# Performance work log

Hardware: AMD Instinct MI355X
Metric: run time of the kernel (lower is better)

The kernel has to match this reference:

```python
import jax, jax.numpy as jnp
import numpy as np

N, E = 50000, 400000
C_IN, C_OUT = 64, 32
K = 9  # kernel_size 3x3


def _quad_basis(t):
    # open B-spline basis, degree 2, per torch_spline_conv: k_mod in {0,1,2}
    # t = frac(pseudo * (kernel_size - degree)) = pseudo here (kernel_size=3, degree=2)
    return jnp.stack([0.5 * (1.0 - t) ** 2, -t * t + t + 0.5, 0.5 * t * t], axis=-1)  # [E,3]


def spline_basis(pseudo):
    # kernel_size=[3,3], degree=2, open spline: v = p*(3-2)=p, floor(v)=0 for p in [0,1),
    # so weight index for combination s is exactly s = k_mod0 + 3*k_mod1.
    q0 = _quad_basis(pseudo[:, 0])  # [E,3] varies with s%3
    q1 = _quad_basis(pseudo[:, 1])  # [E,3] varies with s//3
    return (q1[:, :, None] * q0[:, None, :]).reshape(-1, K)  # [E,9]


def spline_conv(x, src, dst, B, W, root, bias, n_nodes):
    xj = x[src]  # gather source node features [E,Cin]
    msg = jnp.zeros((xj.shape[0], W.shape[-1]), x.dtype)
    for k in range(K):  # fixed small kernel loop; avoids [E,K,Cin] blowup
        msg = msg + (xj * B[:, k, None]) @ W[k]
    agg = jax.ops.segment_sum(msg, dst, num_segments=n_nodes)  # aggr='add'
    return agg + x @ root + bias


def setup_inputs() -> dict:
    key = jax.random.key(0)
    ks = jax.random.split(key, 10)
    x = jax.random.normal(ks[0], (N, C_IN), jnp.float32)
    edge_index = jax.random.randint(ks[1], (2, E), 0, N, jnp.int64)
    pseudo = jax.random.uniform(ks[2], (E, 2), jnp.float32)
    skip = jax.random.normal(ks[3], (N, C_OUT), jnp.float32)
    s1 = 1.0 / np.sqrt(C_IN)
    s2 = 1.0 / np.sqrt(C_OUT)
    W1 = jax.random.normal(ks[4], (K, C_IN, C_OUT), jnp.float32) * s1
    root1 = jax.random.normal(ks[5], (C_IN, C_OUT), jnp.float32) * s1
    b1 = jnp.zeros((C_OUT,), jnp.float32)
    W2 = jax.random.normal(ks[6], (K, C_OUT, C_OUT), jnp.float32) * s2
    root2 = jax.random.normal(ks[7], (C_OUT, C_OUT), jnp.float32) * s2
    b2 = jnp.zeros((C_OUT,), jnp.float32)
    return {"x": x, "edge_index": edge_index, "pseudo": pseudo, "skip": skip,
            "W1": W1, "root1": root1, "b1": b1, "W2": W2, "root2": root2, "b2": b2}


def reference(x, edge_index, pseudo, skip, W1, root1, b1, W2, root2, b2):
    src, dst = edge_index[0], edge_index[1]  # flow: source_to_target
    B = spline_basis(pseudo)  # [E,9]
    n = x.shape[0]
    h = jax.nn.relu(spline_conv(x, src, dst, B, W1, root1, b1, n))
    h = jnp.concatenate([h, skip], axis=1)  # [N, Cout+Cskip] == [N, Cin]
    h = jax.nn.relu(spline_conv(h, src, dst, B, W1, root1, b1, n))
    h = jax.nn.relu(spline_conv(h, src, dst, B, W2, root2, b2, n))
    return h
```

## Files before the change

### kernel.cpp

```cpp
#include <hip/hip_runtime.h>
#include <hip/hip_bf16.h>


typedef __attribute__((ext_vector_type(8))) short short8;
typedef __attribute__((ext_vector_type(4))) float f32x4;

__device__ __forceinline__ float blo(unsigned u) {
    union { unsigned u; float f; } x; x.u = u << 16; return x.f;
}
__device__ __forceinline__ float bhi(unsigned u) {
    union { unsigned u; float f; } x; x.u = u & 0xffff0000u; return x.f;
}
__device__ __forceinline__ unsigned short f2bf(float f) {
    union { float f; unsigned u; } x; x.f = f;
    unsigned r = x.u + 0x7fffu + ((x.u >> 16) & 1u);
    return (unsigned short)(r >> 16);
}
__device__ __forceinline__ short8 cvt8(const float* p) {
    float4 a = *(const float4*)p;
    float4 b = *(const float4*)(p + 4);
    short8 r;
    r[0] = (short)f2bf(a.x); r[1] = (short)f2bf(a.y);
    r[2] = (short)f2bf(a.z); r[3] = (short)f2bf(a.w);
    r[4] = (short)f2bf(b.x); r[5] = (short)f2bf(b.y);
    r[6] = (short)f2bf(b.z); r[7] = (short)f2bf(b.w);
    return r;
}

#define YROW 296

__device__ __forceinline__ void m_phase(const unsigned short* sY,
                                        const int* __restrict__ sstart,
                                        const float4* __restrict__ erec,
                                        uint4* __restrict__ msgOut,
                                        int n0, int t, int N, int E)
{
    const int e0 = sstart[n0];
    const int e1 = (n0 + 32 < N) ? sstart[n0 + 32] : E;
    const int l  = t & 3;

    int e = e0 + (t >> 2);
    if (e >= e1) return;
    float4 r = erec[e];
    while (true) {
        const int en = e + 64;
        float4 rn;
        if (en < e1) rn = erec[en];

        const int srcl = __float_as_int(r.x) - n0;
        const int dp   = __float_as_int(r.y);
        const float p0 = r.z, p1 = r.w;

        const float qb[3] = {0.5f * (1.f - p0) * (1.f - p0), -p0 * p0 + p0 + 0.5f, 0.5f * p0 * p0};
        const float qa[3] = {0.5f * (1.f - p1) * (1.f - p1), -p1 * p1 + p1 + 0.5f, 0.5f * p1 * p1};

        const uint4* yb = (const uint4*)(sY + srcl * YROW) + l;
        float s[8] = {0.f, 0.f, 0.f, 0.f, 0.f, 0.f, 0.f, 0.f};
        #pragma unroll
        for (int a = 0; a < 3; ++a) {
            float z[8] = {0.f, 0.f, 0.f, 0.f, 0.f, 0.f, 0.f, 0.f};
            #pragma unroll
            for (int b = 0; b < 3; ++b) {
                uint4 v = yb[(a * 3 + b) * 4];
                const float cw = qb[b];
                z[0] = fmaf(cw, blo(v.x), z[0]); z[1] = fmaf(cw, bhi(v.x), z[1]);
                z[2] = fmaf(cw, blo(v.y), z[2]); z[3] = fmaf(cw, bhi(v.y), z[3]);
                z[4] = fmaf(cw, blo(v.z), z[4]); z[5] = fmaf(cw, bhi(v.z), z[5]);
                z[6] = fmaf(cw, blo(v.w), z[6]); z[7] = fmaf(cw, bhi(v.w), z[7]);
            }
            #pragma unroll
            for (int j = 0; j < 8; ++j) s[j] = fmaf(qa[a], z[j], s[j]);
        }

        union { uint4 u; __hip_bfloat162 h[4]; } o;
        #pragma unroll
        for (int j = 0; j < 4; ++j)
            o.h[j] = __float22bfloat162_rn(float2{s[2 * j], s[2 * j + 1]});
        msgOut[(size_t)dp * 4 + l] = o.u;

        if (en >= e1) break;
        r = rn; e = en;
    }
}

template<int NHALF>
__device__ __forceinline__ void t_core(short8 a0, short8 a1,
                                       const unsigned short* __restrict__ Wt,
                                       const float* __restrict__ bias,
                                       unsigned short* sY, float* __restrict__ aggOut,
                                       int n0, int rh, int cgp, int lc, int q, int N)
{
    const int CIN = NHALF * 32;
    #pragma unroll
    for (int j = 0; j < 10; ++j) {
        const int ti = cgp * 10 + j;
        const unsigned short* wp = Wt + ((size_t)(ti * 16 + lc)) * CIN + q * 8;
        f32x4 acc = (f32x4){0.f, 0.f, 0.f, 0.f};
        acc = __builtin_amdgcn_mfma_f32_16x16x32_bf16(a0, *(const short8*)wp, acc, 0, 0, 0);
        if (NHALF == 2)
            acc = __builtin_amdgcn_mfma_f32_16x16x32_bf16(a1, *(const short8*)(wp + 32), acc, 0, 0, 0);

        if (ti < 18) {
            #pragma unroll
            for (int r = 0; r < 4; ++r) {
                int nl = rh * 16 + q * 4 + r;
                sY[nl * YROW + ti * 16 + lc] = f2bf(acc[r]);
            }
        } else {
            int c = (ti - 18) * 16 + lc;
            float bv = bias[c];
            #pragma unroll
            for (int r = 0; r < 4; ++r) {
                int n = n0 + rh * 16 + q * 4 + r;
                if (n < N) aggOut[(size_t)n * 32 + c] = acc[r] + bv;
            }
        }
    }
}

__global__ __launch_bounds__(256, 8)
void layer_tm0(const float* __restrict__ Xa,
               const unsigned short* __restrict__ Wt, const float* __restrict__ bias,
               const int* __restrict__ sstart, const float4* __restrict__ erec,
               float* __restrict__ aggOut, uint4* __restrict__ msgOut, int N, int E)
{
    __shared__ __align__(16) unsigned short sY[32 * YROW];
    const int t = threadIdx.x, wv = t >> 6, lane = t & 63;
    const int lc = lane & 15, q = lane >> 4;
    const int rh = wv & 1, cgp = wv >> 1;
    const int n0 = blockIdx.x * 32;

    int na = n0 + rh * 16 + lc;
    if (na >= N) na = N - 1;
    const float* p = Xa + (size_t)na * 64 + q * 8;
    short8 a0 = cvt8(p);
    short8 a1 = cvt8(p + 32);

    t_core<2>(a0, a1, Wt, bias, sY, aggOut, n0, rh, cgp, lc, q, N);
    __syncthreads();
    m_phase(sY, sstart, erec, msgOut, n0, t, N, E);
}

template<int MODE>
__global__ __launch_bounds__(256, 8)
void layer_gtm(const float* __restrict__ aggPrev, const float* __restrict__ skipv,
               const unsigned short* __restrict__ Wt, const float* __restrict__ bias,
               const int* __restrict__ sstart, const int* __restrict__ dstart,
               const float4* __restrict__ erec,
               const uint4* __restrict__ msgIn, uint4* __restrict__ msgOut,
               float* __restrict__ aggOut, int N, int E)
{
    __shared__ __align__(16) unsigned short sY[32 * YROW];
    float* sH = (float*)sY;
    const int t = threadIdx.x, wv = t >> 6, lane = t & 63;
    const int lc = lane & 15, q = lane >> 4;
    const int rh = wv & 1, cgp = wv >> 1;
    const int n0 = blockIdx.x * 32;

    {
        const int nl = t >> 3;
        const int l  = t & 3;
        const int h  = (t >> 2) & 1;
        int n = n0 + nl;
        if (n >= N) n = N - 1;
        float4 A, B;
        if (h == 0) {
            const float* ap = aggPrev + (size_t)n * 32 + l * 8;
            A = *(const float4*)ap;
            B = *(const float4*)(ap + 4);
        } else {
            A = {0.f, 0.f, 0.f, 0.f};
            B = {0.f, 0.f, 0.f, 0.f};
        }
        float4 C = {0.f, 0.f, 0.f, 0.f}, D = {0.f, 0.f, 0.f, 0.f};
        const int e0 = dstart[n] - E;
        const int e1 = ((n + 1 < N) ? dstart[n + 1] : 2 * E) - E;
        const uint4* mp = msgIn + l;
        int e = e0 + h;
        for (; e + 2 < e1; e += 4) {
            uint4 v0 = mp[(size_t)e * 4];
            uint4 v1 = mp[(size_t)(e + 2) * 4];
            A.x += blo(v0.x); A.y += bhi(v0.x); A.z += blo(v0.y); A.w += bhi(v0.y);
            B.x += blo(v0.z); B.y += bhi(v0.z); B.z += blo(v0.w); B.w += bhi(v0.w);
            C.x += blo(v1.x); C.y += bhi(v1.x); C.z += blo(v1.y); C.w += bhi(v1.y);
            D.x += blo(v1.z); D.y += bhi(v1.z); D.z += blo(v1.w); D.w += bhi(v1.w);
        }
        if (e < e1) {
            uint4 v = mp[(size_t)e * 4];
            A.x += blo(v.x); A.y += bhi(v.x); A.z += blo(v.y); A.w += bhi(v.y);
            B.x += blo(v.z); B.y += bhi(v.z); B.z += blo(v.w); B.w += bhi(v.w);
        }
        A.x += C.x; A.y += C.y; A.z += C.z; A.w += C.w;
        B.x += D.x; B.y += D.y; B.z += D.z; B.w += D.w;
        A.x += __shfl_xor(A.x, 4); A.y += __shfl_xor(A.y, 4);
        A.z += __shfl_xor(A.z, 4); A.w += __shfl_xor(A.w, 4);
        B.x += __shfl_xor(B.x, 4); B.y += __shfl_xor(B.y, 4);
        B.z += __shfl_xor(B.z, 4); B.w += __shfl_xor(B.w, 4);
        if (h == 0) {
            float* hp = sH + nl * 33 + l * 8;
            hp[0] = fmaxf(A.x, 0.f); hp[1] = fmaxf(A.y, 0.f);
            hp[2] = fmaxf(A.z, 0.f); hp[3] = fmaxf(A.w, 0.f);
            hp[4] = fmaxf(B.x, 0.f); hp[5] = fmaxf(B.y, 0.f);
            hp[6] = fmaxf(B.z, 0.f); hp[7] = fmaxf(B.w, 0.f);
        }
    }
    __syncthreads();

    const float* hp = sH + (rh * 16 + lc) * 33 + q * 8;
    union { short8 v; __hip_bfloat162 h2[4]; } pk;
    #pragma unroll
    for (int j = 0; j < 4; ++j)
        pk.h2[j] = __float22bfloat162_rn(float2{hp[2 * j], hp[2 * j + 1]});
    short8 a0 = pk.v;
    short8 a1;
    if (MODE == 1) {
        int na = n0 + rh * 16 + lc;
        if (na >= N) na = N - 1;
        a1 = cvt8(skipv + (size_t)na * 32 + q * 8);
    }
    __syncthreads();

    t_core<(MODE == 1) ? 2 : 1>(a0, a1, Wt, bias, sY, aggOut, n0, rh, cgp, lc, q, N);
    __syncthreads();
    m_phase(sY, sstart, erec, msgOut, n0, t, N, E);
}

__global__ __launch_bounds__(256)
void gather_kernel(const int* __restrict__ dstart, const uint4* __restrict__ msg4,
                   float* __restrict__ agg, int N, int E)
{
    const int t = threadIdx.x;
    const int n = blockIdx.x * 32 + (t >> 3);
    if (n >= N) return;
    const int l = t & 3;
    const int h = (t >> 2) & 1;

    const int e0 = dstart[n] - E;
    const int e1 = ((n + 1 < N) ? dstart[n + 1] : 2 * E) - E;

    float4* ap = (float4*)(agg + (size_t)n * 32 + l * 8);
    float4 A, B;
    if (h == 0) { A = ap[0]; B = ap[1]; }
    else { A = {0.f, 0.f, 0.f, 0.f}; B = {0.f, 0.f, 0.f, 0.f}; }
    float4 C = {0.f, 0.f, 0.f, 0.f}, D = {0.f, 0.f, 0.f, 0.f};
    const uint4* mp = msg4 + l;
    int e = e0 + h;
    for (; e + 2 < e1; e += 4) {
        uint4 v0 = mp[(size_t)e * 4];
        uint4 v1 = mp[(size_t)(e + 2) * 4];
        A.x += blo(v0.x); A.y += bhi(v0.x); A.z += blo(v0.y); A.w += bhi(v0.y);
        B.x += blo(v0.z); B.y += bhi(v0.z); B.z += blo(v0.w); B.w += bhi(v0.w);
        C.x += blo(v1.x); C.y += bhi(v1.x); C.z += blo(v1.y); C.w += bhi(v1.y);
        D.x += blo(v1.z); D.y += bhi(v1.z); D.z += blo(v1.w); D.w += bhi(v1.w);
    }
    if (e < e1) {
        uint4 v = mp[(size_t)e * 4];
        A.x += blo(v.x); A.y += bhi(v.x); A.z += blo(v.y); A.w += bhi(v.y);
        B.x += blo(v.z); B.y += bhi(v.z); B.z += blo(v.w); B.w += bhi(v.w);
    }
    A.x += C.x; A.y += C.y; A.z += C.z; A.w += C.w;
    B.x += D.x; B.y += D.y; B.z += D.z; B.w += D.w;
    A.x += __shfl_xor(A.x, 4); A.y += __shfl_xor(A.y, 4);
    A.z += __shfl_xor(A.z, 4); A.w += __shfl_xor(A.w, 4);
    B.x += __shfl_xor(B.x, 4); B.y += __shfl_xor(B.y, 4);
    B.z += __shfl_xor(B.z, 4); B.w += __shfl_xor(B.w, 4);
    if (h == 0) {
        A.x = fmaxf(A.x, 0.f); A.y = fmaxf(A.y, 0.f); A.z = fmaxf(A.z, 0.f); A.w = fmaxf(A.w, 0.f);
        B.x = fmaxf(B.x, 0.f); B.y = fmaxf(B.y, 0.f); B.z = fmaxf(B.z, 0.f); B.w = fmaxf(B.w, 0.f);
        ap[0] = A; ap[1] = B;
    }
}


__global__ __launch_bounds__(256)
void init_kernel(int* __restrict__ hist, int n2,
                 const float* __restrict__ W1, const float* __restrict__ root1,
                 const float* __restrict__ W2, const float* __restrict__ root2,
                 unsigned short* __restrict__ Wt1, unsigned short* __restrict__ Wt2)
{
    int i = blockIdx.x * 256 + threadIdx.x;
    if (i < n2) { hist[i] = 0; return; }
    int j = i - n2;
    if (j < 320 * 64) {
        int col = j / 64, k = j % 64;
        float v = (col < 288) ? W1[((size_t)(col >> 5) * 64 + k) * 32 + (col & 31)]
                              : root1[(size_t)k * 32 + (col - 288)];
        Wt1[j] = f2bf(v);
    } else if (j < 320 * 96) {
        int jj = j - 320 * 64;
        int col = jj / 32, k = jj % 32;
        float v = (col < 288) ? W2[((size_t)(col >> 5) * 32 + k) * 32 + (col & 31)]
                              : root2[(size_t)k * 32 + (col - 288)];
        Wt2[jj] = f2bf(v);
    }
}

__global__ __launch_bounds__(256)
void count_rank_kernel(const int* __restrict__ ei, int* __restrict__ hist,
                       uint2* __restrict__ rank, int N, int E)
{
    int e = blockIdx.x * 256 + threadIdx.x;
    if (e >= E) return;
    unsigned rs = atomicAdd((unsigned*)&hist[ei[e]], 1u);
    unsigned rd = atomicAdd((unsigned*)&hist[N + ei[E + e]], 1u);
    rank[e] = uint2{rs, rd};
}

__global__ __launch_bounds__(1024)
void scan1_kernel(int* __restrict__ hist, int* __restrict__ bsum, int n)
{
    __shared__ int s[1024];
    int tid = threadIdx.x;
    int i = blockIdx.x * 1024 + tid;
    int v = (i < n) ? hist[i] : 0;
    s[tid] = v;
    __syncthreads();
    for (int off = 1; off < 1024; off <<= 1) {
        int add = (tid >= off) ? s[tid - off] : 0;
        __syncthreads();
        s[tid] += add;
        __syncthreads();
    }
    if (i < n) hist[i] = s[tid] - v;
    if (tid == 1023) bsum[blockIdx.x] = s[1023];
}

__global__ __launch_bounds__(1024)
void scan3_kernel(int* __restrict__ hist, const int* __restrict__ bsum, int n)
{
    __shared__ int sred[128];
    int tid = threadIdx.x;
    int b = blockIdx.x;
    if (tid < 128) sred[tid] = (tid < b) ? bsum[tid] : 0;
    __syncthreads();
    for (int off = 64; off > 0; off >>= 1) {
        if (tid < off) sred[tid] += sred[tid + off];
        __syncthreads();
    }
    int pre = sred[0];
    int i = b * 1024 + tid;
    if (i < n) hist[i] += pre;
}

__global__ __launch_bounds__(256)
void scatter_plain_kernel(const int* __restrict__ ei, const float* __restrict__ pseudo,
                          const int* __restrict__ start, const uint2* __restrict__ rank,
                          float4* __restrict__ erec, int N, int E)
{
    int e = blockIdx.x * 256 + threadIdx.x;
    if (e >= E) return;
    int sv = ei[e];
    int dv = ei[E + e];
    uint2 rk = rank[e];
    int ps = start[sv] + (int)rk.x;
    int pd = start[N + dv] + (int)rk.y - E;
    float4 r;
    r.x = __int_as_float(sv);
    r.y = __int_as_float(pd);
    r.z = pseudo[2 * (size_t)e];
    r.w = pseudo[2 * (size_t)e + 1];
    erec[ps] = r;
}

extern "C" void kernel_launch(void* const* d_in, const int* in_sizes, int n_in,
                              void* d_out, int out_size, void* d_ws, size_t ws_size,
                              hipStream_t stream) {
    const float* x      = (const float*)d_in[0];
    const int*   ei     = (const int*)  d_in[1];
    const float* pseudo = (const float*)d_in[2];
    const float* skip   = (const float*)d_in[3];
    const float* W1     = (const float*)d_in[4];
    const float* root1  = (const float*)d_in[5];
    const float* b1     = (const float*)d_in[6];
    const float* W2     = (const float*)d_in[7];
    const float* root2  = (const float*)d_in[8];
    const float* b2     = (const float*)d_in[9];

    const int N = in_sizes[0] / 64;
    const int E = in_sizes[1] / 2;
    float* out = (float*)d_out;

    unsigned short* msgA = (unsigned short*)d_ws;
    unsigned short* msgB = msgA + (size_t)E * 32;
    float*  agg1  = (float*)(msgB + (size_t)E * 32);
    float*  agg2  = agg1 + (size_t)N * 32;
    float4* erec  = (float4*)(agg2 + (size_t)N * 32);
    int*    start = (int*)(erec + E);
    int*    bsum  = start + 2 * N;
    unsigned short* Wt1 = (unsigned short*)(bsum + 256);
    unsigned short* Wt2 = Wt1 + 320 * 64;
    uint2*  rank  = (uint2*)msgB;

    const dim3 blk(256);
    const int tb   = (N + 31) / 32;
    const int gb   = (N + 31) / 32;
    const int e256 = (E + 255) / 256;
    const int n2k  = (2 * N + 1023) / 1024;
    const int itot = 2 * N + 320 * 96;
    int* dstart = start + N;

    init_kernel<<<(itot + 255) / 256, blk, 0, stream>>>(start, 2 * N, W1, root1, W2, root2, Wt1, Wt2);
    count_rank_kernel<<<e256, blk, 0, stream>>>(ei, start, rank, N, E);
    scan1_kernel<<<n2k, 1024, 0, stream>>>(start, bsum, 2 * N);
    scan3_kernel<<<n2k, 1024, 0, stream>>>(start, bsum, 2 * N);
    scatter_plain_kernel<<<e256, blk, 0, stream>>>(ei, pseudo, start, rank, erec, N, E);

    layer_tm0<<<tb, blk, 0, stream>>>(x, Wt1, b1, start, erec, agg1, (uint4*)msgA, N, E);
    layer_gtm<1><<<tb, blk, 0, stream>>>(agg1, skip, Wt1, b1, start, dstart, erec,
                                         (const uint4*)msgA, (uint4*)msgB, agg2, N, E);
    layer_gtm<2><<<tb, blk, 0, stream>>>(agg2, nullptr, Wt2, b2, start, dstart, erec,
                                         (const uint4*)msgB, (uint4*)msgA, out, N, E);
    gather_kernel<<<gb, blk, 0, stream>>>(dstart, (const uint4*)msgA, out, N, E);
}
```

Baseline: 226.7 us.

## Write messages in source order and gather via destination-position index

```diff
diff --git a/kernel.cpp b/kernel.cpp
--- a/kernel.cpp
+++ b/kernel.cpp
@@ -48,7 +48,6 @@
         if (en < e1) rn = erec[en];
 
         const int srcl = __float_as_int(r.x) - n0;
-        const int dp   = __float_as_int(r.y);
         const float p0 = r.z, p1 = r.w;
 
         const float qb[3] = {0.5f * (1.f - p0) * (1.f - p0), -p0 * p0 + p0 + 0.5f, 0.5f * p0 * p0};
@@ -76,7 +75,7 @@
         #pragma unroll
         for (int j = 0; j < 4; ++j)
             o.h[j] = __float22bfloat162_rn(float2{s[2 * j], s[2 * j + 1]});
-        msgOut[(size_t)dp * 4 + l] = o.u;
+        msgOut[(size_t)e * 4 + l] = o.u;
 
         if (en >= e1) break;
         r = rn; e = en;
@@ -146,7 +145,7 @@
 void layer_gtm(const float* __restrict__ aggPrev, const float* __restrict__ skipv,
                const unsigned short* __restrict__ Wt, const float* __restrict__ bias,
                const int* __restrict__ sstart, const int* __restrict__ dstart,
-               const float4* __restrict__ erec,
+               const float4* __restrict__ erec, const int* __restrict__ pos,
                const uint4* __restrict__ msgIn, uint4* __restrict__ msgOut,
                float* __restrict__ aggOut, int N, int E)
 {
@@ -176,17 +175,22 @@
         const int e0 = dstart[n] - E;
         const int e1 = ((n + 1 < N) ? dstart[n + 1] : 2 * E) - E;
         const uint4* mp = msgIn + l;
-        int e = e0 + h;
-        for (; e + 2 < e1; e += 4) {
-            uint4 v0 = mp[(size_t)e * 4];
-            uint4 v1 = mp[(size_t)(e + 2) * 4];
+        int g = e0 + h;
+        int pc0 = (g < e1)     ? pos[g]     : 0;
+        int pc1 = (g + 2 < e1) ? pos[g + 2] : 0;
+        for (; g + 2 < e1; g += 4) {
+            int pn0 = (g + 4 < e1) ? pos[g + 4] : 0;
+            int pn1 = (g + 6 < e1) ? pos[g + 6] : 0;
+            uint4 v0 = mp[(size_t)pc0 * 4];
+            uint4 v1 = mp[(size_t)pc1 * 4];
             A.x += blo(v0.x); A.y += bhi(v0.x); A.z += blo(v0.y); A.w += bhi(v0.y);
             B.x += blo(v0.z); B.y += bhi(v0.z); B.z += blo(v0.w); B.w += bhi(v0.w);
             C.x += blo(v1.x); C.y += bhi(v1.x); C.z += blo(v1.y); C.w += bhi(v1.y);
             D.x += blo(v1.z); D.y += bhi(v1.z); D.z += blo(v1.w); D.w += bhi(v1.w);
-        }
-        if (e < e1) {
-            uint4 v = mp[(size_t)e * 4];
+            pc0 = pn0; pc1 = pn1;
+        }
+        if (g < e1) {
+            uint4 v = mp[(size_t)pc0 * 4];
             A.x += blo(v.x); A.y += bhi(v.x); A.z += blo(v.y); A.w += bhi(v.y);
             B.x += blo(v.z); B.y += bhi(v.z); B.z += blo(v.w); B.w += bhi(v.w);
         }
@@ -226,8 +230,8 @@
 }
 
 __global__ __launch_bounds__(256)
-void gather_kernel(const int* __restrict__ dstart, const uint4* __restrict__ msg4,
-                   float* __restrict__ agg, int N, int E)
+void gather_kernel(const int* __restrict__ dstart, const int* __restrict__ pos,
+                   const uint4* __restrict__ msg4, float* __restrict__ agg, int N, int E)
 {
     const int t = threadIdx.x;
     const int n = blockIdx.x * 32 + (t >> 3);
@@ -244,17 +248,22 @@
     else { A = {0.f, 0.f, 0.f, 0.f}; B = {0.f, 0.f, 0.f, 0.f}; }
     float4 C = {0.f, 0.f, 0.f, 0.f}, D = {0.f, 0.f, 0.f, 0.f};
     const uint4* mp = msg4 + l;
-    int e = e0 + h;
-    for (; e + 2 < e1; e += 4) {
-        uint4 v0 = mp[(size_t)e * 4];
-        uint4 v1 = mp[(size_t)(e + 2) * 4];
+    int g = e0 + h;
+    int pc0 = (g < e1)     ? pos[g]     : 0;
+    int pc1 = (g + 2 < e1) ? pos[g + 2] : 0;
+    for (; g + 2 < e1; g += 4) {
+        int pn0 = (g + 4 < e1) ? pos[g + 4] : 0;
+        int pn1 = (g + 6 < e1) ? pos[g + 6] : 0;
+        uint4 v0 = mp[(size_t)pc0 * 4];
+        uint4 v1 = mp[(size_t)pc1 * 4];
         A.x += blo(v0.x); A.y += bhi(v0.x); A.z += blo(v0.y); A.w += bhi(v0.y);
         B.x += blo(v0.z); B.y += bhi(v0.z); B.z += blo(v0.w); B.w += bhi(v0.w);
         C.x += blo(v1.x); C.y += bhi(v1.x); C.z += blo(v1.y); C.w += bhi(v1.y);
         D.x += blo(v1.z); D.y += bhi(v1.z); D.z += blo(v1.w); D.w += bhi(v1.w);
-    }
-    if (e < e1) {
-        uint4 v = mp[(size_t)e * 4];
+        pc0 = pn0; pc1 = pn1;
+    }
+    if (g < e1) {
+        uint4 v = mp[(size_t)pc0 * 4];
         A.x += blo(v.x); A.y += bhi(v.x); A.z += blo(v.y); A.w += bhi(v.y);
         B.x += blo(v.z); B.y += bhi(v.z); B.z += blo(v.w); B.w += bhi(v.w);
     }
@@ -345,7 +354,7 @@
 __global__ __launch_bounds__(256)
 void scatter_plain_kernel(const int* __restrict__ ei, const float* __restrict__ pseudo,
                           const int* __restrict__ start, const uint2* __restrict__ rank,
-                          float4* __restrict__ erec, int N, int E)
+                          float4* __restrict__ erec, int* __restrict__ pos, int N, int E)
 {
     int e = blockIdx.x * 256 + threadIdx.x;
     if (e >= E) return;
@@ -356,10 +365,11 @@
     int pd = start[N + dv] + (int)rk.y - E;
     float4 r;
     r.x = __int_as_float(sv);
-    r.y = __int_as_float(pd);
+    r.y = 0.f;
     r.z = pseudo[2 * (size_t)e];
     r.w = pseudo[2 * (size_t)e + 1];
     erec[ps] = r;
+    pos[pd] = ps;
 }
 
 extern "C" void kernel_launch(void* const* d_in, const int* in_sizes, int n_in,
@@ -389,6 +399,7 @@
     int*    bsum  = start + 2 * N;
     unsigned short* Wt1 = (unsigned short*)(bsum + 256);
     unsigned short* Wt2 = Wt1 + 320 * 64;
+    int*    pos   = (int*)(Wt2 + 320 * 32);
     uint2*  rank  = (uint2*)msgB;
 
     const dim3 blk(256);
@@ -403,12 +414,12 @@
     count_rank_kernel<<<e256, blk, 0, stream>>>(ei, start, rank, N, E);
     scan1_kernel<<<n2k, 1024, 0, stream>>>(start, bsum, 2 * N);
     scan3_kernel<<<n2k, 1024, 0, stream>>>(start, bsum, 2 * N);
-    scatter_plain_kernel<<<e256, blk, 0, stream>>>(ei, pseudo, start, rank, erec, N, E);
+    scatter_plain_kernel<<<e256, blk, 0, stream>>>(ei, pseudo, start, rank, erec, pos, N, E);
 
     layer_tm0<<<tb, blk, 0, stream>>>(x, Wt1, b1, start, erec, agg1, (uint4*)msgA, N, E);
-    layer_gtm<1><<<tb, blk, 0, stream>>>(agg1, skip, Wt1, b1, start, dstart, erec,
+    layer_gtm<1><<<tb, blk, 0, stream>>>(agg1, skip, Wt1, b1, start, dstart, erec, pos,
                                          (const uint4*)msgA, (uint4*)msgB, agg2, N, E);
-    layer_gtm<2><<<tb, blk, 0, stream>>>(agg2, nullptr, Wt2, b2, start, dstart, erec,
+    layer_gtm<2><<<tb, blk, 0, stream>>>(agg2, nullptr, Wt2, b2, start, dstart, erec, pos,
                                          (const uint4*)msgB, (uint4*)msgA, out, N, E);
-    gather_kernel<<<gb, blk, 0, stream>>>(dstart, (const uint4*)msgA, out, N, E);
-}
+    gather_kernel<<<gb, blk, 0, stream>>>(dstart, pos, (const uint4*)msgA, out, N, E);
+}
```

After: 242.7 us. +7.0%, slower.
